# Optimization experiments

Hardware: AMD Instinct MI355X
Metric: run time of the kernel (lower is better)

## Reference

```python
import math
import jax, jax.numpy as jnp
import numpy as np

R, C, D, ORDER = 2048, 2048, 64, 3
O = ORDER + 1  # var_size


def setup_inputs() -> dict:
    key = jax.random.key(0)
    k1, k2, k3, k4, k5, k6 = jax.random.split(key, 6)
    return {
        "events": jax.random.randint(k1, (R, C), 0, 2, dtype=jnp.int32),
        "col_times": jax.random.uniform(k2, (C,), dtype=jnp.float32),
        "z_rows": jax.random.normal(k3, (O, R, D), dtype=jnp.float32),
        "z_cols": jax.random.normal(k4, (C, D), dtype=jnp.float32),
        "gamma_rows": jax.random.uniform(k5, (R,), dtype=jnp.float32),
        "gamma_cols": jax.random.uniform(k6, (C,), dtype=jnp.float32),
    }


def reference(events, col_times, z_rows, z_cols, gamma_rows, gamma_cols):
    o = z_rows.shape[0]
    facts = np.array([math.factorial(i) for i in range(o)], dtype=np.float32)
    # Taylor time-basis: coeffs[o, c] = t_c^o / o!   (replaces nested Python loops)
    coeffs = jnp.stack([col_times ** i for i in range(o)]) / facts[:, None]  # (O, C)
    # row positions at each column's time: (R, C, D)
    pos = jnp.einsum('ord,oc->rcd', z_rows, coeffs)
    diff = pos - z_cols[None, :, :]                        # (R, C, D)
    dist = jnp.sqrt(jnp.sum(diff * diff, axis=-1))         # (R, C) pairwise L2
    logit = gamma_rows[:, None] + gamma_cols[None, :] - dist
    # log p where p = 1 - E - (1-2E)*sigmoid(logit):
    #   E==1 -> log sigmoid(logit); E==0 -> log sigmoid(-logit)
    sign = jnp.where(events == 1, 1.0, -1.0).astype(logit.dtype)
    log_lik = jnp.sum(jax.nn.log_sigmoid(sign * logit))
    return -log_lik
```

## Files before the change

kernel.cpp:

```cpp
#include <hip/hip_runtime.h>
#include <hip/hip_bf16.h>
#include <math.h>

#define R_DIM 2048
#define C_DIM 2048
#define D_DIM 64
#define O_DIM 4
#define K_USED 272
#define K_TOT 288
#define WB_WORDS (C_DIM / 64)

typedef __attribute__((ext_vector_type(8))) short short8;
typedef __attribute__((ext_vector_type(4))) float floatx4;


__device__ __forceinline__ ushort f2bf(float f) {
  unsigned u = __float_as_uint(f);
  return (ushort)((u + 0x7FFFu + ((u >> 16) & 1u)) >> 16);
}

__device__ __forceinline__ void load16_lds(const void* g, void* l) {
  auto gp = reinterpret_cast<const __attribute__((address_space(1))) unsigned int*>(
      reinterpret_cast<uintptr_t>(g));
  auto lp = reinterpret_cast<__attribute__((address_space(3))) unsigned int*>(
      (unsigned int)reinterpret_cast<uintptr_t>(l));
  __builtin_amdgcn_global_load_lds(gp, lp, 16, 0, 0);
}

__global__ void prep_kernel(const int* __restrict__ events,
                            const float* __restrict__ col_times,
                            const float* __restrict__ z_rows,
                            const float* __restrict__ z_cols,
                            ushort* __restrict__ Ab,
                            ushort* __restrict__ Bb,
                            float* __restrict__ nzc,
                            unsigned long long* __restrict__ Wb,
                            float* __restrict__ out) {
  const int b = blockIdx.x;
  const int t = threadIdx.x;
  const int w = t >> 6;
  const int lane = t & 63;

  if (b == 0 && t == 0) out[0] = 0.0f;

  if (b < 512) {
    const int r = b * 4 + w;
    float zv[O_DIM];
#pragma unroll
    for (int o = 0; o < O_DIM; ++o) {
      zv[o] = z_rows[(size_t)(o * R_DIM + r) * D_DIM + lane];
      Ab[(size_t)r * K_TOT + o * 64 + lane] = f2bf(zv[o]);
    }
    float g00 = zv[0] * zv[0], g01 = zv[0] * zv[1], g02 = zv[0] * zv[2],
          g03 = zv[0] * zv[3], g11 = zv[1] * zv[1], g12 = zv[1] * zv[2],
          g13 = zv[1] * zv[3], g22 = zv[2] * zv[2], g23 = zv[2] * zv[3],
          g33 = zv[3] * zv[3];
#pragma unroll
    for (int off = 32; off > 0; off >>= 1) {
      g00 += __shfl_xor(g00, off); g01 += __shfl_xor(g01, off);
      g02 += __shfl_xor(g02, off); g03 += __shfl_xor(g03, off);
      g11 += __shfl_xor(g11, off); g12 += __shfl_xor(g12, off);
      g13 += __shfl_xor(g13, off); g22 += __shfl_xor(g22, off);
      g23 += __shfl_xor(g23, off); g33 += __shfl_xor(g33, off);
    }
    if (lane == 0) {
      ushort* e = Ab + (size_t)r * K_TOT + 256;
      e[0] = f2bf(g00);  e[1] = f2bf(g01);  e[2] = f2bf(g02);  e[3] = f2bf(g03);
      e[4] = f2bf(g01);  e[5] = f2bf(g11);  e[6] = f2bf(g12);  e[7] = f2bf(g13);
      e[8] = f2bf(g02);  e[9] = f2bf(g12);  e[10] = f2bf(g22); e[11] = f2bf(g23);
      e[12] = f2bf(g03); e[13] = f2bf(g13); e[14] = f2bf(g23); e[15] = f2bf(g33);
    }
    if (lane < 16) Ab[(size_t)r * K_TOT + K_USED + lane] = 0;
  } else if (b < 1024) {
    const int c = (b - 512) * 4 + w;
    const float tt = col_times[c];
    float cf[4];
    cf[0] = 1.0f; cf[1] = tt; cf[2] = tt * tt * 0.5f;
    cf[3] = tt * tt * tt * (1.0f / 6.0f);
    const float zc = z_cols[(size_t)c * D_DIM + lane];
#pragma unroll
    for (int o = 0; o < O_DIM; ++o)
      Bb[(size_t)c * K_TOT + o * 64 + lane] = f2bf(-2.0f * cf[o] * zc);
    float q = zc * zc;
#pragma unroll
    for (int off = 32; off > 0; off >>= 1) q += __shfl_xor(q, off);
    if (lane == 0) {
      nzc[c] = q;
      ushort* e = Bb + (size_t)c * K_TOT + 256;
#pragma unroll
      for (int i = 0; i < 16; ++i) e[i] = f2bf(cf[i >> 2] * cf[i & 3]);
    }
    if (lane < 16) Bb[(size_t)c * K_TOT + K_USED + lane] = 0;
  } else {
    const int r = b - 1024;
    const int cbase = w * 512;
#pragma unroll
    for (int i = 0; i < 8; ++i) {
      const int col = cbase + i * 64 + lane;
      const int ev = events[(size_t)r * C_DIM + col];
      const unsigned long long mask = __ballot(ev == 1);
      if (lane == 0) Wb[r * WB_WORDS + (cbase >> 6) + i] = mask;
    }
  }
}

__launch_bounds__(256, 4)
__global__ void pair_kernel(const float* __restrict__ gamma_rows,
                            const float* __restrict__ gamma_cols,
                            const ushort* __restrict__ Ab,
                            const ushort* __restrict__ Bb,
                            const float* __restrict__ nzc,
                            const unsigned long long* __restrict__ Wb,
                            float* __restrict__ out) {
  __shared__ __align__(16) ushort As[64 * 32];
  __shared__ __align__(16) ushort Bs[64 * 32];
  __shared__ float red[4];

  const int t = threadIdx.x;
  const int widx = t >> 6;
  const int lane = t & 63;
  const int m0 = blockIdx.y * 64;
  const int c0 = blockIdx.x * 64;
  const int wm = widx & 1;
  const int wn = widx >> 1;
  const int lm = lane & 15;
  const int kg = lane >> 4;

  floatx4 acc[2][2];
#pragma unroll
  for (int i = 0; i < 2; ++i)
#pragma unroll
    for (int j = 0; j < 2; ++j) acc[i][j] = (floatx4){0.f, 0.f, 0.f, 0.f};

  const int srow = t >> 2;
  const int selem = (t & 3) * 8;

  for (int kt = 0; kt < K_TOT; kt += 32) {
    load16_lds(Ab + (size_t)(m0 + srow) * K_TOT + kt + selem,
               (char*)As + widx * 1024);
    load16_lds(Bb + (size_t)(c0 + srow) * K_TOT + kt + selem,
               (char*)Bs + widx * 1024);
    __syncthreads();

    short8 a[2], b[2];
#pragma unroll
    for (int mt = 0; mt < 2; ++mt)
      a[mt] = *(const short8*)(As + (wm * 32 + mt * 16 + lm) * 32 + kg * 8);
#pragma unroll
    for (int nt = 0; nt < 2; ++nt)
      b[nt] = *(const short8*)(Bs + (wn * 32 + nt * 16 + lm) * 32 + kg * 8);
#pragma unroll
    for (int mt = 0; mt < 2; ++mt)
#pragma unroll
      for (int nt = 0; nt < 2; ++nt)
        acc[mt][nt] = __builtin_amdgcn_mfma_f32_16x16x32_bf16(
            a[mt], b[nt], acc[mt][nt], 0, 0, 0);
    __syncthreads();
  }

  float gc[2], nz[2];
  int cbit[2];
#pragma unroll
  for (int nt = 0; nt < 2; ++nt) {
    const int c = c0 + wn * 32 + nt * 16 + lm;
    gc[nt] = gamma_cols[c];
    nz[nt] = nzc[c];
    cbit[nt] = c & 63;
  }
  const int wword = blockIdx.x;
  float lsum = 0.0f;
#pragma unroll
  for (int mt = 0; mt < 2; ++mt) {
    const int rbase = m0 + wm * 32 + mt * 16 + kg * 4;
#pragma unroll
    for (int j = 0; j < 4; ++j) {
      const int r = rbase + j;
      const float gr = gamma_rows[r];
      const unsigned long long wbits = Wb[r * WB_WORDS + wword];
#pragma unroll
      for (int nt = 0; nt < 2; ++nt) {
        const float d2 = acc[mt][nt][j] + nz[nt];
        const float dist = sqrtf(fmaxf(d2, 0.0f));
        const float logit = gr + gc[nt] - dist;
        const int ev = (int)((wbits >> cbit[nt]) & 1ull);
        const float x = ev ? -logit : logit;
        lsum += fmaxf(x, 0.0f) + __logf(1.0f + __expf(-fabsf(x)));
      }
    }
  }
#pragma unroll
  for (int off = 32; off > 0; off >>= 1) lsum += __shfl_down(lsum, off);
  if (lane == 0) red[widx] = lsum;
  __syncthreads();
  if (t == 0) atomicAdd(out, red[0] + red[1] + red[2] + red[3]);
}

extern "C" void kernel_launch(void* const* d_in, const int* in_sizes, int n_in,
                              void* d_out, int out_size, void* d_ws, size_t ws_size,
                              hipStream_t stream) {
  const int* events = (const int*)d_in[0];
  const float* col_times = (const float*)d_in[1];
  const float* z_rows = (const float*)d_in[2];
  const float* z_cols = (const float*)d_in[3];
  const float* gamma_rows = (const float*)d_in[4];
  const float* gamma_cols = (const float*)d_in[5];
  float* out = (float*)d_out;

  ushort* Ab = (ushort*)d_ws;
  ushort* Bb = Ab + (size_t)R_DIM * K_TOT;
  float* nzc = (float*)(Bb + (size_t)C_DIM * K_TOT);
  unsigned long long* Wb = (unsigned long long*)(nzc + C_DIM);

  prep_kernel<<<3072, 256, 0, stream>>>(events, col_times, z_rows, z_cols, Ab,
                                        Bb, nzc, Wb, out);
  dim3 grid(C_DIM / 64, R_DIM / 64);
  pair_kernel<<<grid, 256, 0, stream>>>(gamma_rows, gamma_cols, Ab, Bb, nzc, Wb,
                                        out);
}
```

Before: 95.49 us.

## Load MFMA operands directly from global and merge prep work per row

The pair kernel drops its LDS staging and the two barriers per K-step, and instead loads bf16 operand fragments straight from global memory into registers for each of the nine K-steps. The prep kernel is collapsed to one block per row/column index. That block packs event bits with int4 loads and shuffles into 32-bit words, and also builds the A and B rows. The log-sigmoid epilogue uses an algebraic form, softplus(logit) - e*logit, in place of the sign select. Launch bounds are relaxed from 4 to 3. The risk is more redundant global or L2 traffic, since each wave now fetches its own operand fragments.

```diff
diff --git a/kernel.cpp b/kernel.cpp
--- a/kernel.cpp
+++ b/kernel.cpp
@@ -5,26 +5,14 @@
 #define R_DIM 2048
 #define C_DIM 2048
 #define D_DIM 64
-#define O_DIM 4
-#define K_USED 272
 #define K_TOT 288
-#define WB_WORDS (C_DIM / 64)
 
 typedef __attribute__((ext_vector_type(8))) short short8;
 typedef __attribute__((ext_vector_type(4))) float floatx4;
 
-
 __device__ __forceinline__ ushort f2bf(float f) {
   unsigned u = __float_as_uint(f);
   return (ushort)((u + 0x7FFFu + ((u >> 16) & 1u)) >> 16);
-}
-
-__device__ __forceinline__ void load16_lds(const void* g, void* l) {
-  auto gp = reinterpret_cast<const __attribute__((address_space(1))) unsigned int*>(
-      reinterpret_cast<uintptr_t>(g));
-  auto lp = reinterpret_cast<__attribute__((address_space(3))) unsigned int*>(
-      (unsigned int)reinterpret_cast<uintptr_t>(l));
-  __builtin_amdgcn_global_load_lds(gp, lp, 16, 0, 0);
 }
 
 __global__ void prep_kernel(const int* __restrict__ events,
@@ -34,22 +22,37 @@
                             ushort* __restrict__ Ab,
                             ushort* __restrict__ Bb,
                             float* __restrict__ nzc,
-                            unsigned long long* __restrict__ Wb,
+                            unsigned* __restrict__ Wb,
                             float* __restrict__ out) {
   const int b = blockIdx.x;
   const int t = threadIdx.x;
-  const int w = t >> 6;
   const int lane = t & 63;
 
   if (b == 0 && t == 0) out[0] = 0.0f;
 
-  if (b < 512) {
-    const int r = b * 4 + w;
-    float zv[O_DIM];
+  const int4 e0 = *(const int4*)&events[(size_t)b * C_DIM + t * 4];
+  const int4 e1 = *(const int4*)&events[(size_t)b * C_DIM + 1024 + t * 4];
+  {
+    unsigned w0 = ((unsigned)(e0.x & 1) | ((unsigned)(e0.y & 1) << 1) |
+                   ((unsigned)(e0.z & 1) << 2) | ((unsigned)(e0.w & 1) << 3))
+                  << ((t & 7) * 4);
+    w0 |= __shfl_xor((int)w0, 1); w0 |= __shfl_xor((int)w0, 2);
+    w0 |= __shfl_xor((int)w0, 4);
+    if ((t & 7) == 0) Wb[b * 64 + (t >> 3)] = w0;
+    unsigned w1 = ((unsigned)(e1.x & 1) | ((unsigned)(e1.y & 1) << 1) |
+                   ((unsigned)(e1.z & 1) << 2) | ((unsigned)(e1.w & 1) << 3))
+                  << ((t & 7) * 4);
+    w1 |= __shfl_xor((int)w1, 1); w1 |= __shfl_xor((int)w1, 2);
+    w1 |= __shfl_xor((int)w1, 4);
+    if ((t & 7) == 0) Wb[b * 64 + 32 + (t >> 3)] = w1;
+  }
+
+  if (t < 64) {
+    float zv[4];
 #pragma unroll
-    for (int o = 0; o < O_DIM; ++o) {
-      zv[o] = z_rows[(size_t)(o * R_DIM + r) * D_DIM + lane];
-      Ab[(size_t)r * K_TOT + o * 64 + lane] = f2bf(zv[o]);
+    for (int o = 0; o < 4; ++o) {
+      zv[o] = z_rows[(size_t)(o * R_DIM + b) * D_DIM + lane];
+      Ab[(size_t)b * K_TOT + o * 64 + lane] = f2bf(zv[o]);
     }
     float g00 = zv[0] * zv[0], g01 = zv[0] * zv[1], g02 = zv[0] * zv[2],
           g03 = zv[0] * zv[3], g11 = zv[1] * zv[1], g12 = zv[1] * zv[2],
@@ -64,67 +67,54 @@
       g23 += __shfl_xor(g23, off); g33 += __shfl_xor(g33, off);
     }
     if (lane == 0) {
-      ushort* e = Ab + (size_t)r * K_TOT + 256;
+      ushort* e = Ab + (size_t)b * K_TOT + 256;
       e[0] = f2bf(g00);  e[1] = f2bf(g01);  e[2] = f2bf(g02);  e[3] = f2bf(g03);
       e[4] = f2bf(g01);  e[5] = f2bf(g11);  e[6] = f2bf(g12);  e[7] = f2bf(g13);
       e[8] = f2bf(g02);  e[9] = f2bf(g12);  e[10] = f2bf(g22); e[11] = f2bf(g23);
       e[12] = f2bf(g03); e[13] = f2bf(g13); e[14] = f2bf(g23); e[15] = f2bf(g33);
     }
-    if (lane < 16) Ab[(size_t)r * K_TOT + K_USED + lane] = 0;
-  } else if (b < 1024) {
-    const int c = (b - 512) * 4 + w;
-    const float tt = col_times[c];
+    if (lane < 16) Ab[(size_t)b * K_TOT + 272 + lane] = 0;
+  } else if (t < 128) {
+    const float tt = col_times[b];
     float cf[4];
     cf[0] = 1.0f; cf[1] = tt; cf[2] = tt * tt * 0.5f;
-    cf[3] = tt * tt * tt * (1.0f / 6.0f);
-    const float zc = z_cols[(size_t)c * D_DIM + lane];
+    cf[3] = cf[2] * tt * (1.0f / 3.0f);
+    const float zc = z_cols[(size_t)b * D_DIM + lane];
 #pragma unroll
-    for (int o = 0; o < O_DIM; ++o)
-      Bb[(size_t)c * K_TOT + o * 64 + lane] = f2bf(-2.0f * cf[o] * zc);
+    for (int o = 0; o < 4; ++o)
+      Bb[(size_t)b * K_TOT + o * 64 + lane] = f2bf(-2.0f * cf[o] * zc);
     float q = zc * zc;
 #pragma unroll
     for (int off = 32; off > 0; off >>= 1) q += __shfl_xor(q, off);
     if (lane == 0) {
-      nzc[c] = q;
-      ushort* e = Bb + (size_t)c * K_TOT + 256;
+      nzc[b] = q;
+      ushort* e = Bb + (size_t)b * K_TOT + 256;
 #pragma unroll
       for (int i = 0; i < 16; ++i) e[i] = f2bf(cf[i >> 2] * cf[i & 3]);
     }
-    if (lane < 16) Bb[(size_t)c * K_TOT + K_USED + lane] = 0;
-  } else {
-    const int r = b - 1024;
-    const int cbase = w * 512;
-#pragma unroll
-    for (int i = 0; i < 8; ++i) {
-      const int col = cbase + i * 64 + lane;
-      const int ev = events[(size_t)r * C_DIM + col];
-      const unsigned long long mask = __ballot(ev == 1);
-      if (lane == 0) Wb[r * WB_WORDS + (cbase >> 6) + i] = mask;
-    }
+    if (lane < 16) Bb[(size_t)b * K_TOT + 272 + lane] = 0;
   }
 }
 
-__launch_bounds__(256, 4)
+__launch_bounds__(256, 3)
 __global__ void pair_kernel(const float* __restrict__ gamma_rows,
                             const float* __restrict__ gamma_cols,
                             const ushort* __restrict__ Ab,
                             const ushort* __restrict__ Bb,
                             const float* __restrict__ nzc,
-                            const unsigned long long* __restrict__ Wb,
+                            const unsigned* __restrict__ Wb,
                             float* __restrict__ out) {
-  __shared__ __align__(16) ushort As[64 * 32];
-  __shared__ __align__(16) ushort Bs[64 * 32];
   __shared__ float red[4];
+  const int t = threadIdx.x;
+  const int widx = t >> 6, lane = t & 63;
+  const int m0 = blockIdx.y * 64, c0 = blockIdx.x * 64;
+  const int wm = widx & 1, wn = widx >> 1;
+  const int lm = lane & 15, kg = lane >> 4;
 
-  const int t = threadIdx.x;
-  const int widx = t >> 6;
-  const int lane = t & 63;
-  const int m0 = blockIdx.y * 64;
-  const int c0 = blockIdx.x * 64;
-  const int wm = widx & 1;
-  const int wn = widx >> 1;
-  const int lm = lane & 15;
-  const int kg = lane >> 4;
+  const ushort* a0p = Ab + (size_t)(m0 + wm * 32 + lm) * K_TOT + kg * 8;
+  const ushort* a1p = a0p + 16 * K_TOT;
+  const ushort* b0p = Bb + (size_t)(c0 + wn * 32 + lm) * K_TOT + kg * 8;
+  const ushort* b1p = b0p + 16 * K_TOT;
 
   floatx4 acc[2][2];
 #pragma unroll
@@ -132,59 +122,37 @@
 #pragma unroll
     for (int j = 0; j < 2; ++j) acc[i][j] = (floatx4){0.f, 0.f, 0.f, 0.f};
 
-  const int srow = t >> 2;
-  const int selem = (t & 3) * 8;
-
-  for (int kt = 0; kt < K_TOT; kt += 32) {
-    load16_lds(Ab + (size_t)(m0 + srow) * K_TOT + kt + selem,
-               (char*)As + widx * 1024);
-    load16_lds(Bb + (size_t)(c0 + srow) * K_TOT + kt + selem,
-               (char*)Bs + widx * 1024);
-    __syncthreads();
-
-    short8 a[2], b[2];
 #pragma unroll
-    for (int mt = 0; mt < 2; ++mt)
-      a[mt] = *(const short8*)(As + (wm * 32 + mt * 16 + lm) * 32 + kg * 8);
-#pragma unroll
-    for (int nt = 0; nt < 2; ++nt)
-      b[nt] = *(const short8*)(Bs + (wn * 32 + nt * 16 + lm) * 32 + kg * 8);
-#pragma unroll
-    for (int mt = 0; mt < 2; ++mt)
-#pragma unroll
-      for (int nt = 0; nt < 2; ++nt)
-        acc[mt][nt] = __builtin_amdgcn_mfma_f32_16x16x32_bf16(
-            a[mt], b[nt], acc[mt][nt], 0, 0, 0);
-    __syncthreads();
+  for (int kt = 0; kt < 9; ++kt) {
+    const short8 a0 = *(const short8*)(a0p + kt * 32);
+    const short8 a1 = *(const short8*)(a1p + kt * 32);
+    const short8 b0 = *(const short8*)(b0p + kt * 32);
+    const short8 b1 = *(const short8*)(b1p + kt * 32);
+    acc[0][0] = __builtin_amdgcn_mfma_f32_16x16x32_bf16(a0, b0, acc[0][0], 0, 0, 0);
+    acc[0][1] = __builtin_amdgcn_mfma_f32_16x16x32_bf16(a0, b1, acc[0][1], 0, 0, 0);
+    acc[1][0] = __builtin_amdgcn_mfma_f32_16x16x32_bf16(a1, b0, acc[1][0], 0, 0, 0);
+    acc[1][1] = __builtin_amdgcn_mfma_f32_16x16x32_bf16(a1, b1, acc[1][1], 0, 0, 0);
   }
 
-  float gc[2], nz[2];
-  int cbit[2];
+  float lsum = 0.0f;
 #pragma unroll
   for (int nt = 0; nt < 2; ++nt) {
     const int c = c0 + wn * 32 + nt * 16 + lm;
-    gc[nt] = gamma_cols[c];
-    nz[nt] = nzc[c];
-    cbit[nt] = c & 63;
-  }
-  const int wword = blockIdx.x;
-  float lsum = 0.0f;
+    const float gc = gamma_cols[c];
+    const float nz = nzc[c];
+    const int cword = c >> 5, cbit = c & 31;
 #pragma unroll
-  for (int mt = 0; mt < 2; ++mt) {
-    const int rbase = m0 + wm * 32 + mt * 16 + kg * 4;
+    for (int mt = 0; mt < 2; ++mt) {
+      const int rbase = m0 + wm * 32 + mt * 16 + kg * 4;
 #pragma unroll
-    for (int j = 0; j < 4; ++j) {
-      const int r = rbase + j;
-      const float gr = gamma_rows[r];
-      const unsigned long long wbits = Wb[r * WB_WORDS + wword];
-#pragma unroll
-      for (int nt = 0; nt < 2; ++nt) {
-        const float d2 = acc[mt][nt][j] + nz[nt];
+      for (int j = 0; j < 4; ++j) {
+        const int r = rbase + j;
+        const float evf = (float)((Wb[r * 64 + cword] >> cbit) & 1u);
+        const float d2 = acc[mt][nt][j] + nz;
         const float dist = sqrtf(fmaxf(d2, 0.0f));
-        const float logit = gr + gc[nt] - dist;
-        const int ev = (int)((wbits >> cbit[nt]) & 1ull);
-        const float x = ev ? -logit : logit;
-        lsum += fmaxf(x, 0.0f) + __logf(1.0f + __expf(-fabsf(x)));
+        const float logit = gamma_rows[r] + gc - dist;
+        lsum += fmaxf(logit, 0.0f) + __logf(1.0f + __expf(-fabsf(logit))) -
+                evf * logit;
       }
     }
   }
@@ -209,10 +177,10 @@
   ushort* Ab = (ushort*)d_ws;
   ushort* Bb = Ab + (size_t)R_DIM * K_TOT;
   float* nzc = (float*)(Bb + (size_t)C_DIM * K_TOT);
-  unsigned long long* Wb = (unsigned long long*)(nzc + C_DIM);
+  unsigned* Wb = (unsigned*)(nzc + C_DIM);
 
-  prep_kernel<<<3072, 256, 0, stream>>>(events, col_times, z_rows, z_cols, Ab,
-                                        Bb, nzc, Wb, out);
+  prep_kernel<<<R_DIM, 256, 0, stream>>>(events, col_times, z_rows, z_cols, Ab,
+                                         Bb, nzc, Wb, out);
   dim3 grid(C_DIM / 64, R_DIM / 64);
   pair_kernel<<<grid, 256, 0, stream>>>(gamma_rows, gamma_cols, Ab, Bb, nzc, Wb,
                                         out);
```

After: 96.72 us. No clear change (+1.3%).
